# Kernel tuning notes

Hardware: AMD Instinct MI355X
Metric: run time of the kernel (lower is better)

Reference implementation:

```python
import jax, jax.numpy as jnp
import numpy as np

N = 100000
E = 1280000
C = 64
MID = 256
OUT = 64
BN_EPS = 1e-5


def setup_inputs() -> dict:
    key = jax.random.key(0)
    ks = jax.random.split(key, 8)
    x = jax.random.normal(ks[0], (N, C), dtype=jnp.float32)
    edge_index = jax.random.randint(ks[1], (2, E), 0, N, dtype=jnp.int64)
    edge_attr = jax.random.normal(ks[2], (E, 1), dtype=jnp.float32)
    batch = jnp.zeros((N,), dtype=jnp.int64)
    # MLP params: Lin(2C->MID), BatchNorm1d(MID), Lin(MID->OUT)
    W1 = jax.random.normal(ks[3], (2 * C, MID), dtype=jnp.float32) / np.sqrt(2 * C)
    b1 = jnp.zeros((MID,), dtype=jnp.float32)
    gamma = jnp.ones((MID,), dtype=jnp.float32)
    beta = jnp.zeros((MID,), dtype=jnp.float32)
    W2 = jax.random.normal(ks[4], (MID, OUT), dtype=jnp.float32) / np.sqrt(MID)
    b2 = jnp.zeros((OUT,), dtype=jnp.float32)
    return {"x": x, "edge_index": edge_index, "edge_attr": edge_attr, "batch": batch,
            "W1": W1, "b1": b1, "gamma": gamma, "beta": beta, "W2": W2, "b2": b2}


def reference(x, edge_index, edge_attr, batch, W1, b1, gamma, beta, W2, b2):
    n = x.shape[0]
    row, col = edge_index[0], edge_index[1]
    xc = x[col]                                  # [E, C] irregular gather
    feat = jnp.concatenate([xc, xc * edge_attr], axis=1)  # [E, 2C]
    sums = jax.ops.segment_sum(feat, row, num_segments=n)  # [N, 2C]
    cnt = jax.ops.segment_sum(jnp.ones((feat.shape[0],), feat.dtype), row, num_segments=n)
    agg = sums / jnp.maximum(cnt, 1.0)[:, None]  # scatter_mean
    # MLP: Lin -> ReLU -> BatchNorm1d (training stats) -> Lin
    h = jax.nn.relu(agg @ W1 + b1)
    mu = jnp.mean(h, axis=0)
    var = jnp.var(h, axis=0)                     # biased var, as torch BN uses
    h = (h - mu) * jax.lax.rsqrt(var + BN_EPS) * gamma + beta
    return h @ W2 + b2
```

## Files before the change

### kernel.cpp

```cpp
#include <hip/hip_runtime.h>
#include <hip/hip_bf16.h>

#define MIDF 256
#define OUTF 64
#define CF 64
#define TWO_C 128
#define BN_EPS 1e-5f
#define BCAP 1024
#define NBMAX 1600
#define AGG_LD 136
#define OB_LD 264

typedef __attribute__((ext_vector_type(8))) short bf16x8;
typedef __attribute__((ext_vector_type(4))) float f32x4;

__device__ __forceinline__ ushort f2bf(float f) {
  union { float f; unsigned u; } v; v.f = f;
  return (ushort)((v.u + 0x7fffu + ((v.u >> 16) & 1u)) >> 16);
}
__device__ __forceinline__ float bf2f(unsigned u16) {
  union { unsigned u; float f; } v; v.u = u16 << 16;
  return v.f;
}

__global__ __launch_bounds__(1024) void k_init(int* __restrict__ gcur,
                                               float* __restrict__ bnacc, int NB) {
  int i = threadIdx.x;
  for (; i < NB; i += 1024) gcur[i] = i * BCAP;
  for (i = threadIdx.x; i < 2048; i += 1024) bnacc[i] = 0.f;
}

__global__ __launch_bounds__(1024) void k_front(const int* __restrict__ ei,
    const float* __restrict__ ea, int* __restrict__ gcur, uint2* __restrict__ ebt,
    int E, int NB, int nchunks,
    const float4* __restrict__ xp, uint4* __restrict__ xb, int n8,
    const float* __restrict__ W1, ushort* __restrict__ W1t) {
  __shared__ int lh[NBMAX];
  __shared__ int lb[NBMAX];
  int tid = threadIdx.x;
  if ((int)blockIdx.x == (int)gridDim.x - 1) {
    for (int i = tid; i < TWO_C * MIDF; i += 1024) {
      int c = i & (MIDF - 1), k = i >> 8;
      W1t[(size_t)c * TWO_C + k] = f2bf(W1[(size_t)k * MIDF + c]);
    }
    return;
  }
  if ((int)blockIdx.x >= nchunks) {
    int nb2 = gridDim.x - 1 - nchunks;
    int i = ((int)blockIdx.x - nchunks) * 1024 + tid;
    int st = nb2 * 1024;
    for (; i < n8; i += st) {
      float4 a = xp[2 * i], b = xp[2 * i + 1];
      uint4 o;
      o.x = (unsigned)f2bf(a.x) | ((unsigned)f2bf(a.y) << 16);
      o.y = (unsigned)f2bf(a.z) | ((unsigned)f2bf(a.w) << 16);
      o.z = (unsigned)f2bf(b.x) | ((unsigned)f2bf(b.y) << 16);
      o.w = (unsigned)f2bf(b.z) | ((unsigned)f2bf(b.w) << 16);
      xb[i] = o;
    }
    return;
  }
  int c0 = blockIdx.x * 4096;
  for (int b = tid; b < NB; b += 1024) lh[b] = 0;
  __syncthreads();
  int rows[4];
#pragma unroll
  for (int j = 0; j < 4; ++j) {
    int e = c0 + j * 1024 + tid;
    int r = (e < E) ? ei[e] : -1;
    rows[j] = r;
    if (r >= 0) atomicAdd(&lh[r >> 6], 1);
  }
  __syncthreads();
  for (int b = tid; b < NB; b += 1024) {
    int c = lh[b];
    lb[b] = (c > 0) ? atomicAdd(&gcur[b], c) : 0;
  }
  __syncthreads();
#pragma unroll
  for (int j = 0; j < 4; ++j) {
    int r = rows[j];
    if (r >= 0) {
      int e = c0 + j * 1024 + tid;
      int pos = atomicAdd(&lb[r >> 6], 1);
      ebt[pos] = make_uint2((unsigned)ei[E + e] | ((unsigned)(r & 63) << 20),
                            __float_as_uint(ea[e]));
    }
  }
}

__global__ __launch_bounds__(512, 4) void k_fused(const ushort* __restrict__ xb,
    const uint2* __restrict__ ebt, const int* __restrict__ gcur,
    const ushort* __restrict__ W1t, const float* __restrict__ b1,
    ushort* __restrict__ h, float* __restrict__ bnacc, int n, int NB) {
  __shared__ uint2 recs[BCAP];
  __shared__ ushort aggT[64 * AGG_LD];
  __shared__ ushort obuf[64 * OB_LD];
  __shared__ int hist[64], cbase[64], cursor[64];
  int tid = threadIdx.x;
  int w = tid >> 6, lane = tid & 63;
  int q = lane >> 4, l16 = lane & 15;
  bf16x8 Bf[2][4];
  float bias[2];
#pragma unroll
  for (int c2 = 0; c2 < 2; ++c2) {
    int col = w * 32 + c2 * 16 + l16;
#pragma unroll
    for (int ks = 0; ks < 4; ++ks)
      Bf[c2][ks] = *(const bf16x8*)(W1t + (size_t)col * TWO_C + ks * 32 + q * 8);
    bias[c2] = b1[col];
  }
  float s_sum = 0.f, s_sq = 0.f;
  int c_stat = tid & 255, rb2 = tid >> 8;
  for (int b = blockIdx.x; b < NB; b += gridDim.x) {
    int base = b * BCAP;
    int r0 = b << 6;
    int cnt = gcur[b] - base;
    cnt = min(cnt, BCAP);
    if (tid < 64) hist[tid] = 0;
    __syncthreads();
    uint2 e0 = make_uint2(0u, 0u), e1 = make_uint2(0u, 0u);
    bool v0 = tid < cnt, v1 = 512 + tid < cnt;
    if (v0) e0 = ebt[base + tid];
    if (v1) e1 = ebt[base + 512 + tid];
    if (v0) atomicAdd(&hist[(e0.x >> 20) & 63], 1);
    if (v1) atomicAdd(&hist[(e1.x >> 20) & 63], 1);
    __syncthreads();
    if (tid < 64) {
      int v = hist[tid];
      int sc = v;
#pragma unroll
      for (int d = 1; d < 64; d <<= 1) {
        int t = __shfl_up(sc, d);
        if (tid >= d) sc += t;
      }
      cbase[tid] = sc - v;
      cursor[tid] = sc - v;
    }
    __syncthreads();
    if (v0) {
      int pos = atomicAdd(&cursor[(e0.x >> 20) & 63], 1);
      recs[pos] = make_uint2(e0.x & 0xFFFFF, e0.y);
    }
    if (v1) {
      int pos = atomicAdd(&cursor[(e1.x >> 20) & 63], 1);
      recs[pos] = make_uint2(e1.x & 0xFFFFF, e1.y);
    }
    __syncthreads();
#pragma unroll
    for (int j = 0; j < 8; ++j) {
      int rl = w * 8 + j;
      int s = cbase[rl], d = hist[rl];
      int e = s + d;
      float s0 = 0.f, s1 = 0.f, s2 = 0.f, s3 = 0.f;
      float t0 = 0.f, t1 = 0.f, t2 = 0.f, t3 = 0.f;
      int i = s + q;
      for (; i + 4 < e; i += 8) {
        uint2 pa = recs[i], pb = recs[i + 4];
        uint2 xa = *(const uint2*)(xb + (size_t)pa.x * CF + 4 * l16);
        uint2 xc = *(const uint2*)(xb + (size_t)pb.x * CF + 4 * l16);
        float wa = __uint_as_float(pa.y), wb = __uint_as_float(pb.y);
        float a0 = bf2f(xa.x & 0xffff), a1 = bf2f(xa.x >> 16);
        float a2 = bf2f(xa.y & 0xffff), a3 = bf2f(xa.y >> 16);
        float b0 = bf2f(xc.x & 0xffff), b1v = bf2f(xc.x >> 16);
        float b2v = bf2f(xc.y & 0xffff), b3 = bf2f(xc.y >> 16);
        s0 += a0 + b0; s1 += a1 + b1v; s2 += a2 + b2v; s3 += a3 + b3;
        t0 += a0 * wa + b0 * wb; t1 += a1 * wa + b1v * wb;
        t2 += a2 * wa + b2v * wb; t3 += a3 * wa + b3 * wb;
      }
      if (i < e) {
        uint2 p = recs[i];
        uint2 xv = *(const uint2*)(xb + (size_t)p.x * CF + 4 * l16);
        float wt = __uint_as_float(p.y);
        float a0 = bf2f(xv.x & 0xffff), a1 = bf2f(xv.x >> 16);
        float a2 = bf2f(xv.y & 0xffff), a3 = bf2f(xv.y >> 16);
        s0 += a0; s1 += a1; s2 += a2; s3 += a3;
        t0 += a0 * wt; t1 += a1 * wt; t2 += a2 * wt; t3 += a3 * wt;
      }
      s0 += __shfl_xor(s0, 16); s1 += __shfl_xor(s1, 16);
      s2 += __shfl_xor(s2, 16); s3 += __shfl_xor(s3, 16);
      t0 += __shfl_xor(t0, 16); t1 += __shfl_xor(t1, 16);
      t2 += __shfl_xor(t2, 16); t3 += __shfl_xor(t3, 16);
      s0 += __shfl_xor(s0, 32); s1 += __shfl_xor(s1, 32);
      s2 += __shfl_xor(s2, 32); s3 += __shfl_xor(s3, 32);
      t0 += __shfl_xor(t0, 32); t1 += __shfl_xor(t1, 32);
      t2 += __shfl_xor(t2, 32); t3 += __shfl_xor(t3, 32);
      float inv = 1.0f / fmaxf((float)d, 1.0f);
      if (q == 0) {
        uint2 o;
        o.x = (unsigned)f2bf(s0 * inv) | ((unsigned)f2bf(s1 * inv) << 16);
        o.y = (unsigned)f2bf(s2 * inv) | ((unsigned)f2bf(s3 * inv) << 16);
        *(uint2*)(aggT + rl * AGG_LD + 4 * l16) = o;
        uint2 p2;
        p2.x = (unsigned)f2bf(t0 * inv) | ((unsigned)f2bf(t1 * inv) << 16);
        p2.y = (unsigned)f2bf(t2 * inv) | ((unsigned)f2bf(t3 * inv) << 16);
        *(uint2*)(aggT + rl * AGG_LD + CF + 4 * l16) = p2;
      }
    }
    __syncthreads();
    f32x4 acc[4][2];
#pragma unroll
    for (int rt = 0; rt < 4; ++rt)
#pragma unroll
      for (int c2 = 0; c2 < 2; ++c2) acc[rt][c2] = (f32x4){0.f, 0.f, 0.f, 0.f};
#pragma unroll
    for (int rt = 0; rt < 4; ++rt) {
      bf16x8 Af[4];
#pragma unroll
      for (int ks = 0; ks < 4; ++ks)
        Af[ks] = *(const bf16x8*)(aggT + (size_t)(rt * 16 + l16) * AGG_LD + ks * 32 + q * 8);
#pragma unroll
      for (int ks = 0; ks < 4; ++ks)
#pragma unroll
        for (int c2 = 0; c2 < 2; ++c2)
          acc[rt][c2] = __builtin_amdgcn_mfma_f32_16x16x32_bf16(Af[ks], Bf[c2][ks], acc[rt][c2], 0, 0, 0);
    }
#pragma unroll
    for (int rt = 0; rt < 4; ++rt)
#pragma unroll
      for (int c2 = 0; c2 < 2; ++c2)
#pragma unroll
        for (int r = 0; r < 4; ++r) {
          float vv = fmaxf(acc[rt][c2][r] + bias[c2], 0.f);
          obuf[(rt * 16 + q * 4 + r) * OB_LD + w * 32 + c2 * 16 + l16] = f2bf(vv);
        }
    __syncthreads();
#pragma unroll
    for (int half = 0; half < 2; ++half) {
      int row = (tid >> 4) + half * 32;
      int seg = tid & 15;
      int gr = r0 + row;
      if (gr < n) {
        const uint4* src = (const uint4*)(obuf + row * OB_LD + seg * 16);
        uint4* dst = (uint4*)(h + (size_t)gr * MIDF + seg * 16);
        dst[0] = src[0];
        dst[1] = src[1];
      }
    }
#pragma unroll 4
    for (int r = 0; r < 32; ++r) {
      int rr = rb2 * 32 + r;
      if (r0 + rr < n) {
        float vv = bf2f(obuf[rr * OB_LD + c_stat]);
        s_sum += vv;
        s_sq += vv * vv;
      }
    }
    __syncthreads();
  }
  float* red = (float*)obuf;
  red[tid] = s_sum;
  red[512 + tid] = s_sq;
  __syncthreads();
  int cpy = (blockIdx.x & 3) * 512;
  if (tid < 256) {
    atomicAdd(&bnacc[cpy + tid], red[tid] + red[256 + tid]);
  } else {
    int c = tid - 256;
    atomicAdd(&bnacc[cpy + 256 + c], red[512 + c] + red[768 + c]);
  }
}

__global__ __launch_bounds__(256) void k_final(const float* __restrict__ bnacc,
    const float* __restrict__ gamma, const float* __restrict__ beta,
    const float* __restrict__ W2, const float* __restrict__ b2,
    float* __restrict__ W2p, float* __restrict__ b2p, float invN) {
  __shared__ float scb[MIDF], shb[MIDF], red[256];
  int tid = threadIdx.x;
  float s = bnacc[tid] + bnacc[512 + tid] + bnacc[1024 + tid] + bnacc[1536 + tid];
  float qv = bnacc[256 + tid] + bnacc[768 + tid] + bnacc[1280 + tid] + bnacc[1792 + tid];
  float mu = s * invN;
  float var = qv * invN - mu * mu;
  float sc = gamma[tid] * rsqrtf(var + BN_EPS);
  scb[tid] = sc;
  shb[tid] = beta[tid] - mu * sc;
  __syncthreads();
  float sp = 0.f;
  for (int i = tid; i < MIDF * OUTF; i += 256) {
    int k = i >> 6;
    float wv = W2[i];
    W2p[i] = scb[k] * wv;
    sp += shb[k] * wv;
  }
  red[tid] = sp;
  __syncthreads();
  if (tid < 64)
    b2p[tid] = b2[tid] + red[tid] + red[64 + tid] + red[128 + tid] + red[192 + tid];
}

__global__ __launch_bounds__(256, 2) void k_gemm2(const ushort* __restrict__ h,
    const float* __restrict__ W2p, const float* __restrict__ b2p,
    float* __restrict__ out, int n, int ntiles) {
  int tid = threadIdx.x, w = tid >> 6, lane = tid & 63;
  int q = lane >> 4, l16 = lane & 15;
  bf16x8 Bf[4][8];
#pragma unroll
  for (int ct = 0; ct < 4; ++ct)
#pragma unroll
    for (int ks = 0; ks < 8; ++ks) {
      int c = ct * 16 + l16;
      int k0 = ks * 32 + q * 8;
#pragma unroll
      for (int j = 0; j < 8; ++j)
        Bf[ct][ks][j] = (short)f2bf(W2p[(size_t)(k0 + j) * OUTF + c]);
    }
  float bias[4];
#pragma unroll
  for (int ct = 0; ct < 4; ++ct) bias[ct] = b2p[ct * 16 + l16];
  __shared__ float tile[64 * 68];
  for (int t = blockIdx.x; t < ntiles; t += gridDim.x) {
    int r0 = t * 64;
    int myrow = r0 + w * 16 + l16;
    f32x4 acc[4];
#pragma unroll
    for (int ct = 0; ct < 4; ++ct) acc[ct] = (f32x4){0.f, 0.f, 0.f, 0.f};
#pragma unroll
    for (int ks = 0; ks < 8; ++ks) {
      bf16x8 av;
#pragma unroll
      for (int j = 0; j < 8; ++j) av[j] = 0;
      if (myrow < n) av = *(const bf16x8*)(h + (size_t)myrow * MIDF + ks * 32 + q * 8);
#pragma unroll
      for (int ct = 0; ct < 4; ++ct)
        acc[ct] = __builtin_amdgcn_mfma_f32_16x16x32_bf16(av, Bf[ct][ks], acc[ct], 0, 0, 0);
    }
    __syncthreads();
#pragma unroll
    for (int ct = 0; ct < 4; ++ct)
#pragma unroll
      for (int r = 0; r < 4; ++r)
        tile[(w * 16 + q * 4 + r) * 68 + ct * 16 + l16] = acc[ct][r] + bias[ct];
    __syncthreads();
    int row = tid >> 2, co = (tid & 3) * 16;
    int gr = r0 + row;
    if (gr < n) {
      const float4* src = (const float4*)(tile + row * 68 + co);
      float4* dst = (float4*)(out + (size_t)gr * OUTF + co);
      dst[0] = src[0];
      dst[1] = src[1];
      dst[2] = src[2];
      dst[3] = src[3];
    }
  }
}

extern "C" void kernel_launch(void* const* d_in, const int* in_sizes, int n_in,
                              void* d_out, int out_size, void* d_ws, size_t ws_size,
                              hipStream_t stream) {
  const float* x     = (const float*)d_in[0];
  const int*   ei    = (const int*)d_in[1];
  const float* ea    = (const float*)d_in[2];
  const float* W1    = (const float*)d_in[4];
  const float* b1    = (const float*)d_in[5];
  const float* gamma = (const float*)d_in[6];
  const float* beta  = (const float*)d_in[7];
  const float* W2    = (const float*)d_in[8];
  const float* b2    = (const float*)d_in[9];
  float* out = (float*)d_out;
  int E = in_sizes[2];
  int n = in_sizes[3];
  int NB = (n + 63) >> 6;

  char* ws = (char*)d_ws;
  ushort* h   = (ushort*)ws;
  ushort* xb  = h + (size_t)n * MIDF;
  uint2* ebt  = (uint2*)(xb + (size_t)n * CF);
  ushort* W1t = (ushort*)(ebt + (size_t)NBMAX * BCAP);
  float* W2p  = (float*)(W1t + TWO_C * MIDF);
  float* b2p  = W2p + MIDF * OUTF;
  int* gcur   = (int*)(b2p + 64);
  float* bnacc= (float*)(gcur + NBMAX);

  int nchunks = (E + 4095) / 4096;
  hipLaunchKernelGGL(k_init, dim3(1), dim3(1024), 0, stream, gcur, bnacc, NB);
  hipLaunchKernelGGL(k_front, dim3(nchunks + 257), dim3(1024), 0, stream,
                     ei, ea, gcur, ebt, E, NB, nchunks,
                     (const float4*)x, (uint4*)xb, n * CF / 8, W1, W1t);
  hipLaunchKernelGGL(k_fused, dim3(512), dim3(512), 0, stream,
                     xb, ebt, gcur, W1t, b1, h, bnacc, n, NB);
  hipLaunchKernelGGL(k_final, dim3(1), dim3(256), 0, stream, bnacc, gamma, beta,
                     W2, b2, W2p, b2p, 1.0f / (float)n);
  int nt = (n + 63) / 64;
  hipLaunchKernelGGL(k_gemm2, dim3(512), dim3(256), 0, stream, h, W2p, b2p, out, n, nt);
}
```

Baseline: 249.4 us.

## Store aggregated features instead of hidden layer and recompute first GEMM in back kernel

The fused kernel now writes the 128-wide bf16 aggregate per node instead of the 256-wide hidden activation, computing only BN statistics from register accumulators. The back kernel recomputes Lin1+ReLU from the stored aggregate and then does Lin2, with W2 pre-transposed into bf16 by the final kernel. This halves the intermediate global write/read traffic and removes the obuf shared buffer, letting occupancy and grid size rise. In exchange the first GEMM is done twice, and W1/W2 fragments are reloaded from global memory per tile.

Result: slower. 456.5 us (+83.0%).

```diff
diff --git a/kernel.cpp b/kernel.cpp
--- a/kernel.cpp
+++ b/kernel.cpp
@@ -89,13 +89,12 @@
   }
 }
 
-__global__ __launch_bounds__(512, 4) void k_fused(const ushort* __restrict__ xb,
+__global__ __launch_bounds__(512, 8) void k_fused(const ushort* __restrict__ xb,
     const uint2* __restrict__ ebt, const int* __restrict__ gcur,
     const ushort* __restrict__ W1t, const float* __restrict__ b1,
-    ushort* __restrict__ h, float* __restrict__ bnacc, int n, int NB) {
+    ushort* __restrict__ agg, float* __restrict__ bnacc, int n, int NB) {
   __shared__ uint2 recs[BCAP];
   __shared__ ushort aggT[64 * AGG_LD];
-  __shared__ ushort obuf[64 * OB_LD];
   __shared__ int hist[64], cbase[64], cursor[64];
   int tid = threadIdx.x;
   int w = tid >> 6, lane = tid & 63;
@@ -110,8 +109,7 @@
       Bf[c2][ks] = *(const bf16x8*)(W1t + (size_t)col * TWO_C + ks * 32 + q * 8);
     bias[c2] = b1[col];
   }
-  float s_sum = 0.f, s_sq = 0.f;
-  int c_stat = tid & 255, rb2 = tid >> 8;
+  float bs0 = 0.f, bs1 = 0.f, bq0 = 0.f, bq1 = 0.f;
   for (int b = blockIdx.x; b < NB; b += gridDim.x) {
     int base = b * BCAP;
     int r0 = b << 6;
@@ -198,6 +196,16 @@
       }
     }
     __syncthreads();
+    {
+      int row = tid >> 3, seg = tid & 7;
+      int gr = r0 + row;
+      if (gr < n) {
+        const uint4* src = (const uint4*)(aggT + row * AGG_LD + seg * 16);
+        uint4* dst = (uint4*)(agg + (size_t)gr * TWO_C + seg * 16);
+        dst[0] = src[0];
+        dst[1] = src[1];
+      }
+    }
     f32x4 acc[4][2];
 #pragma unroll
     for (int rt = 0; rt < 4; ++rt)
@@ -218,53 +226,34 @@
 #pragma unroll
     for (int rt = 0; rt < 4; ++rt)
 #pragma unroll
-      for (int c2 = 0; c2 < 2; ++c2)
-#pragma unroll
-        for (int r = 0; r < 4; ++r) {
-          float vv = fmaxf(acc[rt][c2][r] + bias[c2], 0.f);
-          obuf[(rt * 16 + q * 4 + r) * OB_LD + w * 32 + c2 * 16 + l16] = f2bf(vv);
+      for (int r = 0; r < 4; ++r) {
+        int grow = r0 + rt * 16 + q * 4 + r;
+        if (grow < n) {
+          float v0c = fmaxf(acc[rt][0][r] + bias[0], 0.f);
+          float v1c = fmaxf(acc[rt][1][r] + bias[1], 0.f);
+          bs0 += v0c; bq0 += v0c * v0c;
+          bs1 += v1c; bq1 += v1c * v1c;
         }
-    __syncthreads();
-#pragma unroll
-    for (int half = 0; half < 2; ++half) {
-      int row = (tid >> 4) + half * 32;
-      int seg = tid & 15;
-      int gr = r0 + row;
-      if (gr < n) {
-        const uint4* src = (const uint4*)(obuf + row * OB_LD + seg * 16);
-        uint4* dst = (uint4*)(h + (size_t)gr * MIDF + seg * 16);
-        dst[0] = src[0];
-        dst[1] = src[1];
-      }
-    }
-#pragma unroll 4
-    for (int r = 0; r < 32; ++r) {
-      int rr = rb2 * 32 + r;
-      if (r0 + rr < n) {
-        float vv = bf2f(obuf[rr * OB_LD + c_stat]);
-        s_sum += vv;
-        s_sq += vv * vv;
-      }
-    }
-    __syncthreads();
-  }
-  float* red = (float*)obuf;
-  red[tid] = s_sum;
-  red[512 + tid] = s_sq;
-  __syncthreads();
-  int cpy = (blockIdx.x & 3) * 512;
-  if (tid < 256) {
-    atomicAdd(&bnacc[cpy + tid], red[tid] + red[256 + tid]);
-  } else {
-    int c = tid - 256;
-    atomicAdd(&bnacc[cpy + 256 + c], red[512 + c] + red[768 + c]);
+      }
+  }
+  bs0 += __shfl_xor(bs0, 16); bs0 += __shfl_xor(bs0, 32);
+  bq0 += __shfl_xor(bq0, 16); bq0 += __shfl_xor(bq0, 32);
+  bs1 += __shfl_xor(bs1, 16); bs1 += __shfl_xor(bs1, 32);
+  bq1 += __shfl_xor(bq1, 16); bq1 += __shfl_xor(bq1, 32);
+  if (q == 0) {
+    int cpy = ((int)blockIdx.x & 3) * 512;
+    int col0 = w * 32 + l16, col1 = w * 32 + 16 + l16;
+    atomicAdd(&bnacc[cpy + col0], bs0);
+    atomicAdd(&bnacc[cpy + 256 + col0], bq0);
+    atomicAdd(&bnacc[cpy + col1], bs1);
+    atomicAdd(&bnacc[cpy + 256 + col1], bq1);
   }
 }
 
 __global__ __launch_bounds__(256) void k_final(const float* __restrict__ bnacc,
     const float* __restrict__ gamma, const float* __restrict__ beta,
     const float* __restrict__ W2, const float* __restrict__ b2,
-    float* __restrict__ W2p, float* __restrict__ b2p, float invN) {
+    ushort* __restrict__ W2pt, float* __restrict__ b2p, float invN) {
   __shared__ float scb[MIDF], shb[MIDF], red[256];
   int tid = threadIdx.x;
   float s = bnacc[tid] + bnacc[512 + tid] + bnacc[1024 + tid] + bnacc[1536 + tid];
@@ -277,9 +266,9 @@
   __syncthreads();
   float sp = 0.f;
   for (int i = tid; i < MIDF * OUTF; i += 256) {
-    int k = i >> 6;
+    int k = i >> 6, c = i & 63;
     float wv = W2[i];
-    W2p[i] = scb[k] * wv;
+    W2pt[(size_t)c * MIDF + k] = f2bf(scb[k] * wv);
     sp += shb[k] * wv;
   }
   red[tid] = sp;
@@ -288,59 +277,75 @@
     b2p[tid] = b2[tid] + red[tid] + red[64 + tid] + red[128 + tid] + red[192 + tid];
 }
 
-__global__ __launch_bounds__(256, 2) void k_gemm2(const ushort* __restrict__ h,
-    const float* __restrict__ W2p, const float* __restrict__ b2p,
+__global__ __launch_bounds__(256, 4) void k_back(const ushort* __restrict__ agg,
+    const ushort* __restrict__ W1t, const float* __restrict__ b1,
+    const ushort* __restrict__ W2pt, const float* __restrict__ b2p,
     float* __restrict__ out, int n, int ntiles) {
+  __shared__ ushort hT[64 * OB_LD];
   int tid = threadIdx.x, w = tid >> 6, lane = tid & 63;
   int q = lane >> 4, l16 = lane & 15;
-  bf16x8 Bf[4][8];
-#pragma unroll
-  for (int ct = 0; ct < 4; ++ct)
-#pragma unroll
-    for (int ks = 0; ks < 8; ++ks) {
-      int c = ct * 16 + l16;
-      int k0 = ks * 32 + q * 8;
-#pragma unroll
-      for (int j = 0; j < 8; ++j)
-        Bf[ct][ks][j] = (short)f2bf(W2p[(size_t)(k0 + j) * OUTF + c]);
-    }
-  float bias[4];
-#pragma unroll
-  for (int ct = 0; ct < 4; ++ct) bias[ct] = b2p[ct * 16 + l16];
-  __shared__ float tile[64 * 68];
+  float bias1[4], b2b[4];
+#pragma unroll
+  for (int ct = 0; ct < 4; ++ct) {
+    bias1[ct] = b1[w * 64 + ct * 16 + l16];
+    b2b[ct] = b2p[ct * 16 + l16];
+  }
   for (int t = blockIdx.x; t < ntiles; t += gridDim.x) {
     int r0 = t * 64;
-    int myrow = r0 + w * 16 + l16;
-    f32x4 acc[4];
-#pragma unroll
-    for (int ct = 0; ct < 4; ++ct) acc[ct] = (f32x4){0.f, 0.f, 0.f, 0.f};
+    bf16x8 Af[4][4];
+#pragma unroll
+    for (int rt = 0; rt < 4; ++rt) {
+      int row = r0 + rt * 16 + l16;
+      bool ok = row < n;
+#pragma unroll
+      for (int ks = 0; ks < 4; ++ks) {
+        bf16x8 v;
+#pragma unroll
+        for (int j = 0; j < 8; ++j) v[j] = 0;
+        if (ok) v = *(const bf16x8*)(agg + (size_t)row * TWO_C + ks * 32 + q * 8);
+        Af[rt][ks] = v;
+      }
+    }
+#pragma unroll
+    for (int ct = 0; ct < 4; ++ct) {
+      f32x4 acc1[4];
+#pragma unroll
+      for (int rt = 0; rt < 4; ++rt) acc1[rt] = (f32x4){0.f, 0.f, 0.f, 0.f};
+#pragma unroll
+      for (int ks = 0; ks < 4; ++ks) {
+        bf16x8 Bv = *(const bf16x8*)(W1t + (size_t)(w * 64 + ct * 16 + l16) * TWO_C + ks * 32 + q * 8);
+#pragma unroll
+        for (int rt = 0; rt < 4; ++rt)
+          acc1[rt] = __builtin_amdgcn_mfma_f32_16x16x32_bf16(Af[rt][ks], Bv, acc1[rt], 0, 0, 0);
+      }
+#pragma unroll
+      for (int rt = 0; rt < 4; ++rt)
+#pragma unroll
+        for (int r = 0; r < 4; ++r)
+          hT[(rt * 16 + q * 4 + r) * OB_LD + w * 64 + ct * 16 + l16] =
+              f2bf(fmaxf(acc1[rt][r] + bias1[ct], 0.f));
+    }
+    __syncthreads();
+    f32x4 acc2[4];
+#pragma unroll
+    for (int ct = 0; ct < 4; ++ct) acc2[ct] = (f32x4){0.f, 0.f, 0.f, 0.f};
 #pragma unroll
     for (int ks = 0; ks < 8; ++ks) {
-      bf16x8 av;
-#pragma unroll
-      for (int j = 0; j < 8; ++j) av[j] = 0;
-      if (myrow < n) av = *(const bf16x8*)(h + (size_t)myrow * MIDF + ks * 32 + q * 8);
-#pragma unroll
-      for (int ct = 0; ct < 4; ++ct)
-        acc[ct] = __builtin_amdgcn_mfma_f32_16x16x32_bf16(av, Bf[ct][ks], acc[ct], 0, 0, 0);
-    }
-    __syncthreads();
+      bf16x8 A2 = *(const bf16x8*)(hT + (size_t)(w * 16 + l16) * OB_LD + ks * 32 + q * 8);
+#pragma unroll
+      for (int ct = 0; ct < 4; ++ct) {
+        bf16x8 Bv = *(const bf16x8*)(W2pt + (size_t)(ct * 16 + l16) * MIDF + ks * 32 + q * 8);
+        acc2[ct] = __builtin_amdgcn_mfma_f32_16x16x32_bf16(A2, Bv, acc2[ct], 0, 0, 0);
+      }
+    }
 #pragma unroll
     for (int ct = 0; ct < 4; ++ct)
 #pragma unroll
-      for (int r = 0; r < 4; ++r)
-        tile[(w * 16 + q * 4 + r) * 68 + ct * 16 + l16] = acc[ct][r] + bias[ct];
-    __syncthreads();
-    int row = tid >> 2, co = (tid & 3) * 16;
-    int gr = r0 + row;
-    if (gr < n) {
-      const float4* src = (const float4*)(tile + row * 68 + co);
-      float4* dst = (float4*)(out + (size_t)gr * OUTF + co);
-      dst[0] = src[0];
-      dst[1] = src[1];
-      dst[2] = src[2];
-      dst[3] = src[3];
-    }
+      for (int r = 0; r < 4; ++r) {
+        int gr = r0 + w * 16 + q * 4 + r;
+        if (gr < n) out[(size_t)gr * OUTF + ct * 16 + l16] = acc2[ct][r] + b2b[ct];
+      }
+    __syncthreads();
   }
 }
 
@@ -362,24 +367,25 @@
   int NB = (n + 63) >> 6;
 
   char* ws = (char*)d_ws;
-  ushort* h   = (ushort*)ws;
-  ushort* xb  = h + (size_t)n * MIDF;
-  uint2* ebt  = (uint2*)(xb + (size_t)n * CF);
-  ushort* W1t = (ushort*)(ebt + (size_t)NBMAX * BCAP);
-  float* W2p  = (float*)(W1t + TWO_C * MIDF);
-  float* b2p  = W2p + MIDF * OUTF;
-  int* gcur   = (int*)(b2p + 64);
-  float* bnacc= (float*)(gcur + NBMAX);
+  ushort* agg  = (ushort*)ws;
+  ushort* xb   = agg + (size_t)n * TWO_C;
+  uint2* ebt   = (uint2*)(xb + (size_t)n * CF);
+  ushort* W1t  = (ushort*)(ebt + (size_t)NBMAX * BCAP);
+  ushort* W2pt = W1t + TWO_C * MIDF;
+  float* b2p   = (float*)(W2pt + MIDF * OUTF);
+  int* gcur    = (int*)(b2p + 64);
+  float* bnacc = (float*)(gcur + NBMAX);
 
   int nchunks = (E + 4095) / 4096;
   hipLaunchKernelGGL(k_init, dim3(1), dim3(1024), 0, stream, gcur, bnacc, NB);
   hipLaunchKernelGGL(k_front, dim3(nchunks + 257), dim3(1024), 0, stream,
                      ei, ea, gcur, ebt, E, NB, nchunks,
                      (const float4*)x, (uint4*)xb, n * CF / 8, W1, W1t);
-  hipLaunchKernelGGL(k_fused, dim3(512), dim3(512), 0, stream,
-                     xb, ebt, gcur, W1t, b1, h, bnacc, n, NB);
+  hipLaunchKernelGGL(k_fused, dim3(1024), dim3(512), 0, stream,
+                     xb, ebt, gcur, W1t, b1, agg, bnacc, n, NB);
   hipLaunchKernelGGL(k_final, dim3(1), dim3(256), 0, stream, bnacc, gamma, beta,
-                     W2, b2, W2p, b2p, 1.0f / (float)n);
+                     W2, b2, W2pt, b2p, 1.0f / (float)n);
   int nt = (n + 63) / 64;
-  hipLaunchKernelGGL(k_gemm2, dim3(512), dim3(256), 0, stream, h, W2p, b2p, out, n, nt);
-}
+  hipLaunchKernelGGL(k_back, dim3(1024), dim3(256), 0, stream,
+                     agg, W1t, b1, W2pt, b2p, out, n, nt);
+}
```
